# Optimization experiments

Measured on AMD Instinct MI355X. Metric: run time of the kernel, lower is better.

The kernel has to match this reference:

```python
import jax, jax.numpy as jnp
import numpy as np

NARROW = 127.0                      # narrow int8 range [-127, 127]
ACT_SCALE = 6.0 / 127.0             # fixed stand-in for learned ActQuant per-tensor scale
FLOW_SCALE = 3.96875 / 127.0        # ConstFlowQuant: max_val 3.96875, 8-bit narrow


def ste_round(x):
    # straight-through rounding (Brevitas-style)
    return x + jax.lax.stop_gradient(jnp.round(x) - x)


def act_quant(x, scale):
    # per-tensor narrow int8 fake-quant (quantize -> clamp -> dequantize)
    return scale * jnp.clip(ste_round(x / scale), -NARROW, NARROW)


def weight_quant(w):
    # per-tensor stats-based narrow int8 weight fake-quant
    s = jax.lax.stop_gradient(jnp.max(jnp.abs(w))) / NARROW + 1e-12
    return s * jnp.clip(ste_round(w / s), -NARROW, NARROW)


def conv2d(x, w, b, groups=1, pad=0):
    y = jax.lax.conv_general_dilated(
        x, w, window_strides=(1, 1), padding=[(pad, pad), (pad, pad)],
        dimension_numbers=("NCHW", "OIHW", "NCHW"), feature_group_count=groups)
    return y + b[None, :, None, None]


def setup_inputs() -> dict:
    key = jax.random.key(0)
    ks = jax.random.split(key, 12)
    B, H, W = 8, 120, 160
    cor_planes = 4 * (2 * 3 + 1) ** 2  # 196
    return {
        "flow": jax.random.normal(ks[0], (B, 2, H, W), jnp.float32),
        "corr": jax.random.normal(ks[1], (B, cor_planes, H, W), jnp.float32),
        "Wc1": jax.random.normal(ks[2], (96, cor_planes, 1, 1), jnp.float32) * 0.05,
        "bc1": jax.random.normal(ks[3], (96,), jnp.float32) * 0.05,
        "Wf1": jax.random.normal(ks[4], (64, 2, 1, 1), jnp.float32) * 0.05,
        "bf1": jax.random.normal(ks[5], (64,), jnp.float32) * 0.05,
        "Wf2": jax.random.normal(ks[6], (32, 64, 1, 1), jnp.float32) * 0.05,
        "bf2": jax.random.normal(ks[7], (32,), jnp.float32) * 0.05,
        "Wd": jax.random.normal(ks[8], (128, 1, 3, 3), jnp.float32) * 0.05,
        "bd": jax.random.normal(ks[9], (128,), jnp.float32) * 0.05,
        "Wp": jax.random.normal(ks[10], (80, 128, 1, 1), jnp.float32) * 0.05,
        "bp": jax.random.normal(ks[11], (80,), jnp.float32) * 0.05,
    }


def reference(flow, corr, Wc1, bc1, Wf1, bf1, Wf2, bf2, Wd, bd, Wp, bp):
    # convc1: 1x1 quant conv with output ActQuant, then ReLU
    cor = jax.nn.relu(act_quant(conv2d(corr, weight_quant(Wc1), bc1), ACT_SCALE))
    # convf1: 1x1 quant conv (no output quant), ReLU
    flo = jax.nn.relu(conv2d(flow, weight_quant(Wf1), bf1))
    # convf2: input ActQuant, 1x1 conv, output quant (shared with convc1), ReLU
    flo = jax.nn.relu(act_quant(conv2d(act_quant(flo, ACT_SCALE), weight_quant(Wf2), bf2), ACT_SCALE))
    # QuantCat with ConstFlowQuant on inputs and output -> [B,128,H,W]
    cor_flo = act_quant(
        jnp.concatenate([act_quant(cor, FLOW_SCALE), act_quant(flo, FLOW_SCALE)], axis=1),
        FLOW_SCALE)
    # depthwise 3x3 quant conv (groups=128), input ActQuant
    d = conv2d(act_quant(cor_flo, ACT_SCALE), weight_quant(Wd), bd, groups=128, pad=1)
    # pointwise 1x1 quant conv, input ActQuant, ReLU
    out = jax.nn.relu(conv2d(act_quant(d, ACT_SCALE), weight_quant(Wp), bp))
    # final QuantCat(out, flow) with ConstFlowQuant -> [B,82,H,W]
    return act_quant(
        jnp.concatenate([act_quant(out, FLOW_SCALE), act_quant(flow, FLOW_SCALE)], axis=1),
        FLOW_SCALE)
```

## Files before the change

kernel.cpp:

```cpp
#include <hip/hip_runtime.h>
#include <hip/hip_bf16.h>
#include <cstddef>

#define BB   8
#define HH   120
#define WW   160
#define HW   19200
#define NPIX 153600
#define CORC 196

#define AS_  ((float)(6.0/127.0))
#define FS_  0.03125f

#define OFF_WF1 18832
#define OFF_WF2 18960
#define OFF_WD  21008
#define OFF_WPQ_US 44320
#define CFQ_BYTE_OFF 131072

typedef __attribute__((ext_vector_type(8)))  short short8;
typedef __attribute__((ext_vector_type(4)))  float f32x4;

__device__ __forceinline__ float clip127(float x) {
    return fminf(fmaxf(x, -127.f), 127.f);
}

__device__ __forceinline__ unsigned short f2bf(float x) {
    unsigned int u = __float_as_uint(x);
    unsigned int r = (u + 0x7fffu + ((u >> 16) & 1u)) >> 16;
    return (unsigned short)r;
}

__global__ __launch_bounds__(256) void quant_weights(
    const float* __restrict__ Wc1, const float* __restrict__ Wf1,
    const float* __restrict__ Wf2, const float* __restrict__ Wd,
    const float* __restrict__ Wp,  float* __restrict__ ws)
{
    __shared__ float red[256];
    const int t = blockIdx.x;
    const float* src = (t == 0) ? Wc1 : (t == 1) ? Wf1 : (t == 2) ? Wf2 : (t == 3) ? Wd : Wp;
    const int n = (t == 0) ? 18816 : (t == 1) ? 128 : (t == 2) ? 2048 : (t == 3) ? 1152 : 10240;
    const int tid = threadIdx.x;

    float m = 0.f;
    for (int i = tid; i < n; i += 256) m = fmaxf(m, fabsf(src[i]));
    red[tid] = m;
    __syncthreads();
    for (int s = 128; s > 0; s >>= 1) {
        if (tid < s) red[tid] = fmaxf(red[tid], red[tid + s]);
        __syncthreads();
    }
    const float s = red[0] / 127.0f + 1e-12f;

    if (t == 0) {
        unsigned short* bf = (unsigned short*)ws + 32;
        for (int j = tid; j < 21504; j += 256) {
            const int e    = j & 7;
            const int l    = (j >> 3) & 63;
            const int tile = j >> 9;
            const int nt   = tile % 6;
            const int kt   = tile / 6;
            const int out  = nt * 16 + (l & 15);
            const int k    = kt * 32 + ((l >> 4) << 3) + e;
            float q = 0.f;
            if (k < 196) q = clip127(rintf(Wc1[out * 196 + k] / s));
            bf[j] = f2bf(q);
        }
        if (tid == 0) ws[2] = s;
    } else if (t == 4) {
        unsigned short* bf = (unsigned short*)ws + OFF_WPQ_US;
        for (int j = tid; j < 10240; j += 256) {
            const int e    = j & 7;
            const int l    = (j >> 3) & 63;
            const int tile = j >> 9;
            const int nt   = tile % 5;
            const int kt   = tile / 5;
            const int o    = nt * 16 + (l & 15);
            const int k    = kt * 32 + ((l >> 4) << 3) + e;
            const float q  = clip127(rintf(Wp[o * 128 + k] / s));
            bf[j] = f2bf(q);
        }
        if (tid == 0) ws[1] = s;
    } else {
        for (int i = tid; i < n; i += 256) {
            const float q = clip127(rintf(src[i] / s));
            if (t == 1) {
                ws[OFF_WF1 + i] = s * q;
            } else if (t == 2) {
                int o = i / 64, c = i % 64;
                ws[OFF_WF2 + c * 32 + o] = s * q;
            } else {
                ws[OFF_WD + i] = q;
            }
        }
        if (tid == 0 && t == 3) ws[0] = s;
    }
}

#define LDSTRIDE 232
__global__ __launch_bounds__(256) void k1_convc1(
    const float* __restrict__ corr, const float* __restrict__ bc1,
    const float* __restrict__ ws,   signed char* __restrict__ cfq)
{
    __shared__ unsigned short hbuf[64 * LDSTRIDE];
    __shared__ unsigned short lbuf[64 * LDSTRIDE];

    const int tid = threadIdx.x;
    const int p0  = blockIdx.x * 64;
    const int b   = p0 / HW;
    const int hw0 = p0 % HW;
    const float* cp = corr + (size_t)b * CORC * HW + hw0;

    const int pix  = tid & 63;
    const int cgrp = tid >> 6;
    unsigned short* hrow = hbuf + pix * LDSTRIDE;
    unsigned short* lrow = lbuf + pix * LDSTRIDE;

    for (int iter = 0; iter < 13; ++iter) {
        const int c0 = iter * 16 + cgrp * 4;
        unsigned long long hp = 0ull, lp = 0ull;
#pragma unroll
        for (int j = 0; j < 4; ++j) {
            const int c = c0 + j;
            float a = 0.f;
            if (c < 196) a = cp[(size_t)c * HW + pix];
            const unsigned short h = f2bf(a);
            const float hf = __uint_as_float((unsigned int)h << 16);
            const unsigned short lo = f2bf(a - hf);
            hp |= (unsigned long long)h  << (16 * j);
            lp |= (unsigned long long)lo << (16 * j);
        }
        *(unsigned long long*)(hrow + c0) = hp;
        *(unsigned long long*)(lrow + c0) = lp;
    }
    {
        const int c0z = 208 + cgrp * 4;
        *(unsigned long long*)(hrow + c0z) = 0ull;
        *(unsigned long long*)(lrow + c0z) = 0ull;
    }
    __syncthreads();

    const int w = tid >> 6;
    const int l = tid & 63;
    const int arow = w * 16 + (l & 15);
    const int koff = (l >> 4) << 3;
    const unsigned short* hA = hbuf + arow * LDSTRIDE + koff;
    const unsigned short* lA = lbuf + arow * LDSTRIDE + koff;
    const short8* Bfr = (const short8*)((const unsigned short*)ws + 32);

    f32x4 ac0 = {0.f,0.f,0.f,0.f}, ac1 = ac0, ac2 = ac0, ac3 = ac0, ac4 = ac0, ac5 = ac0;

#define NTSTEP(ACC, KT, NT)                                                      \
    {   short8 bq = Bfr[((KT) * 6 + (NT)) * 64 + l];                             \
        ACC = __builtin_amdgcn_mfma_f32_16x16x32_bf16(al_, bq, ACC, 0, 0, 0);    \
        ACC = __builtin_amdgcn_mfma_f32_16x16x32_bf16(ah_, bq, ACC, 0, 0, 0);    }

#pragma unroll
    for (int kt = 0; kt < 7; ++kt) {
        short8 ah_ = *(const short8*)(hA + kt * 32);
        short8 al_ = *(const short8*)(lA + kt * 32);
        NTSTEP(ac0, kt, 0) NTSTEP(ac1, kt, 1) NTSTEP(ac2, kt, 2)
        NTSTEP(ac3, kt, 3) NTSTEP(ac4, kt, 4) NTSTEP(ac5, kt, 5)
    }
#undef NTSTEP

    const float sc1 = ws[2];
    __syncthreads();
    signed char* t8 = (signed char*)hbuf;

#define EPI(ACC, NT)                                                             \
    {   const int out = (NT) * 16 + (l & 15);                                    \
        const float bias = bc1[out];                                             \
        _Pragma("unroll")                                                        \
        for (int i = 0; i < 4; ++i) {                                            \
            const int prow = w * 16 + ((l >> 4) << 2) + i;                       \
            float v  = fmaf(sc1, ACC[i], bias);                                  \
            float aq = AS_ * clip127(rintf(v / AS_));                            \
            float r  = fmaxf(aq, 0.f);                                           \
            float kk = fminf(rintf(r * 32.f), 127.f);                            \
            float cf = kk * FS_;                                                 \
            float q8 = clip127(rintf(cf / AS_));                                 \
            t8[out * 64 + prow] = (signed char)(int)q8;                          \
        }                                                                        }
    EPI(ac0, 0) EPI(ac1, 1) EPI(ac2, 2) EPI(ac3, 3) EPI(ac4, 4) EPI(ac5, 5)
#undef EPI
    __syncthreads();

    const unsigned int* t32 = (const unsigned int*)t8;
#pragma unroll
    for (int r = 0; r < 6; ++r) {
        const int d   = r * 256 + tid;
        const int out = d >> 4;
        const int pd  = d & 15;
        *(unsigned int*)(cfq + (size_t)(b * 128 + out) * HW + hw0 + pd * 4) = t32[d];
    }
}

typedef __attribute__((ext_vector_type(16))) float f32x16;
__global__ __launch_bounds__(256) void k1_flo(
    const float* __restrict__ flow, const float* __restrict__ bf1,
    const float* __restrict__ bf2,  const float* __restrict__ ws,
    signed char* __restrict__ cfq)
{
    const int p  = blockIdx.x * 256 + threadIdx.x;
    const int b  = p / HW;
    const int hw = p % HW;

    const float f0 = flow[(size_t)(b * 2) * HW + hw];
    const float f1 = flow[(size_t)(b * 2 + 1) * HW + hw];

    f32x16 a2a, a2b;
#pragma unroll
    for (int j = 0; j < 16; ++j) { a2a[j] = 0.f; a2b[j] = 0.f; }

    for (int c = 0; c < 64; ++c) {
        const float w0 = ws[OFF_WF1 + 2 * c];
        const float w1 = ws[OFF_WF1 + 2 * c + 1];
        float v  = fmaf(f0, w0, fmaf(f1, w1, bf1[c]));
        float r  = fmaxf(v, 0.f);
        float af = AS_ * fminf(rintf(r / AS_), 127.f);
        const float* w2 = ws + OFF_WF2 + c * 32;
#pragma unroll
        for (int j = 0; j < 16; ++j) {
            a2a[j] = fmaf(af, w2[j],      a2a[j]);
            a2b[j] = fmaf(af, w2[16 + j], a2b[j]);
        }
    }

    signed char* op = cfq + (size_t)b * 128 * HW + (size_t)96 * HW + hw;
#define FLOEPI(ACC, BASE)                                                        \
    _Pragma("unroll")                                                            \
    for (int j = 0; j < 16; ++j) {                                               \
        const int o = (BASE) + j;                                                \
        float v  = ACC[j] + bf2[o];                                              \
        float aq = AS_ * clip127(rintf(v / AS_));                                \
        float r  = fmaxf(aq, 0.f);                                               \
        float kk = fminf(rintf(r * 32.f), 127.f);                                \
        float cf = kk * FS_;                                                     \
        float q8 = clip127(rintf(cf / AS_));                                     \
        op[(size_t)o * HW] = (signed char)(int)q8;                               \
    }
    FLOEPI(a2a, 0) FLOEPI(a2b, 16)
#undef FLOEPI
}

#define STG_STRIDE 44
__global__ __launch_bounds__(256) void k2_dwpw(
    const float* __restrict__ flow, const float* __restrict__ bd,
    const float* __restrict__ bp,   const float* __restrict__ ws,
    const signed char* __restrict__ cfq, float* __restrict__ out)
{
    __shared__ signed char stage[4 * 128 * STG_STRIDE];
    __shared__ unsigned short afrag[64 * 136];

    const int tid = threadIdx.x;
    const int bid = blockIdx.x;
    const int b   = bid / 300;
    const int rem = bid % 300;
    const int h0  = (rem / 5) * 2;
    const int w0  = (rem % 5) * 32;

    for (int j = tid; j < 5120; j += 256) {
        const int i   = j % 10;
        const int c   = (j / 10) % 128;
        const int row = j / 1280;
        const int h   = h0 - 1 + row;
        const int wb  = w0 - 4 + 4 * i;
        unsigned int v = 0u;
        if (h >= 0 && h < HH && wb >= 0 && wb <= WW - 4)
            v = *(const unsigned int*)(cfq + ((size_t)(b * 128 + c) * HW + (size_t)h * WW + wb));
        *(unsigned int*)(stage + (row * 128 + c) * STG_STRIDE + i * 4) = v;
    }
    __syncthreads();

    const int c0 = tid & 63;
    const int pg = tid >> 6;
    const float sd = ws[0], sp = ws[1];
    const float ASsd = AS_ * sd;

    float wd0[9], wd1[9];
#pragma unroll
    for (int t9 = 0; t9 < 9; ++t9) {
        wd0[t9] = ws[OFF_WD + c0 * 9 + t9];
        wd1[t9] = ws[OFF_WD + (c0 + 64) * 9 + t9];
    }
    const float bd0 = bd[c0], bd1 = bd[c0 + 64];

#pragma unroll
    for (int pp = 0; pp < 16; ++pp) {
        const int pix = pg * 16 + pp;
        const int r   = pix >> 5;
        const int col = pix & 31;
        float s0 = 0.f, s1 = 0.f;
#pragma unroll
        for (int dy = 0; dy < 3; ++dy) {
            const int rb = (r + dy) * 128;
            const int xb = 3 + col;
#pragma unroll
            for (int dd = 0; dd < 3; ++dd) {
                s0 = fmaf((float)stage[(rb + c0     ) * STG_STRIDE + xb + dd], wd0[dy * 3 + dd], s0);
                s1 = fmaf((float)stage[(rb + c0 + 64) * STG_STRIDE + xb + dd], wd1[dy * 3 + dd], s1);
            }
        }
        const float q0 = clip127(rintf(fmaf(ASsd, s0, bd0) / AS_));
        const float q1 = clip127(rintf(fmaf(ASsd, s1, bd1) / AS_));
        afrag[pix * 136 + c0]      = f2bf(q0);
        afrag[pix * 136 + c0 + 64] = f2bf(q1);
    }
    __syncthreads();

    const int wv = tid >> 6;
    const int l  = tid & 63;
    const unsigned short* A = afrag + (size_t)(wv * 16 + (l & 15)) * 136 + ((l >> 4) << 3);
    const short8* Bfr = (const short8*)((const unsigned short*)ws + OFF_WPQ_US);

    f32x4 pc0 = {0.f,0.f,0.f,0.f}, pc1 = pc0, pc2 = pc0, pc3 = pc0, pc4 = pc0;

#define PTSTEP(ACC, KT, NT)                                                      \
    {   short8 bq = Bfr[((KT) * 5 + (NT)) * 64 + l];                             \
        ACC = __builtin_amdgcn_mfma_f32_16x16x32_bf16(a_, bq, ACC, 0, 0, 0);     }
#pragma unroll
    for (int kt = 0; kt < 4; ++kt) {
        short8 a_ = *(const short8*)(A + kt * 32);
        PTSTEP(pc0, kt, 0) PTSTEP(pc1, kt, 1) PTSTEP(pc2, kt, 2)
        PTSTEP(pc3, kt, 3) PTSTEP(pc4, kt, 4)
    }
#undef PTSTEP

    const float ASsp = AS_ * sp;
    float* ob = out + (size_t)b * 82 * HW;

#define PEPI(ACC, NT)                                                            \
    {   const int o = (NT) * 16 + (l & 15);                                      \
        const float bias = bp[o];                                                \
        _Pragma("unroll")                                                        \
        for (int i = 0; i < 4; ++i) {                                            \
            const int pix = wv * 16 + ((l >> 4) << 2) + i;                       \
            const int hw  = (h0 + (pix >> 5)) * WW + w0 + (pix & 31);            \
            float v = fmaf(ASsp, ACC[i], bias);                                  \
            float r = fmaxf(v, 0.f);                                             \
            float k = fminf(rintf(r * 32.f), 127.f);                             \
            ob[(size_t)o * HW + hw] = k * FS_;                                   \
        }                                                                        }
    PEPI(pc0, 0) PEPI(pc1, 1) PEPI(pc2, 2) PEPI(pc3, 3) PEPI(pc4, 4)
#undef PEPI

    if (tid < 128) {
        const int ch  = tid >> 6;
        const int pix = tid & 63;
        const int hw  = (h0 + (pix >> 5)) * WW + w0 + (pix & 31);
        const float f = flow[(size_t)(b * 2 + ch) * HW + hw];
        const float k = clip127(rintf(f * 32.f));
        ob[(size_t)(80 + ch) * HW + hw] = k * FS_;
    }
}

extern "C" void kernel_launch(void* const* d_in, const int* in_sizes, int n_in,
                              void* d_out, int out_size, void* d_ws, size_t ws_size,
                              hipStream_t stream) {
    const float* flow = (const float*)d_in[0];
    const float* corr = (const float*)d_in[1];
    const float* Wc1  = (const float*)d_in[2];
    const float* bc1  = (const float*)d_in[3];
    const float* Wf1  = (const float*)d_in[4];
    const float* bf1  = (const float*)d_in[5];
    const float* Wf2  = (const float*)d_in[6];
    const float* bf2  = (const float*)d_in[7];
    const float* Wd   = (const float*)d_in[8];
    const float* bd   = (const float*)d_in[9];
    const float* Wp   = (const float*)d_in[10];
    const float* bp   = (const float*)d_in[11];

    float* ws = (float*)d_ws;
    signed char* cfq = (signed char*)d_ws + CFQ_BYTE_OFF;
    float* out = (float*)d_out;

    quant_weights<<<5, 256, 0, stream>>>(Wc1, Wf1, Wf2, Wd, Wp, ws);
    k1_convc1<<<NPIX / 64, 256, 0, stream>>>(corr, bc1, ws, cfq);
    k1_flo<<<NPIX / 256, 256, 0, stream>>>(flow, bf1, bf2, ws, cfq);
    k2_dwpw<<<2400, 256, 0, stream>>>(flow, bd, bp, ws, cfq, out);
}
```

Measured before the change: 179.6 us.

## Load corr directly into MFMA A-fragments and double pixels per block

The convc1 kernel no longer stages the split bf16 hi/lo corr tile in LDS. Each lane loads its A-fragment elements straight from global memory into registers. Each block now covers 128 pixels, with every wave handling two 16-row tiles that share the B fragments, and it uses a small LDS buffer only for the int8 output transpose. This removes about 59KB of LDS and a barrier, which raises occupancy and halves the grid. The cost is strided, less coalesced global loads per lane and more accumulator registers.

```diff
diff --git a/kernel.cpp b/kernel.cpp
--- a/kernel.cpp
+++ b/kernel.cpp
@@ -97,102 +97,86 @@
     }
 }
 
-#define LDSTRIDE 232
-__global__ __launch_bounds__(256) void k1_convc1(
+#define TSTRIDE 136
+__global__ __launch_bounds__(256, 4) void k1_convc1(
     const float* __restrict__ corr, const float* __restrict__ bc1,
     const float* __restrict__ ws,   signed char* __restrict__ cfq)
 {
-    __shared__ unsigned short hbuf[64 * LDSTRIDE];
-    __shared__ unsigned short lbuf[64 * LDSTRIDE];
+    __shared__ signed char t8[96 * TSTRIDE];
 
     const int tid = threadIdx.x;
-    const int p0  = blockIdx.x * 64;
+    const int w   = tid >> 6;
+    const int l   = tid & 63;
+    const int p0  = blockIdx.x * 128;
     const int b   = p0 / HW;
     const int hw0 = p0 % HW;
     const float* cp = corr + (size_t)b * CORC * HW + hw0;
 
-    const int pix  = tid & 63;
-    const int cgrp = tid >> 6;
-    unsigned short* hrow = hbuf + pix * LDSTRIDE;
-    unsigned short* lrow = lbuf + pix * LDSTRIDE;
-
-    for (int iter = 0; iter < 13; ++iter) {
-        const int c0 = iter * 16 + cgrp * 4;
-        unsigned long long hp = 0ull, lp = 0ull;
-#pragma unroll
-        for (int j = 0; j < 4; ++j) {
-            const int c = c0 + j;
-            float a = 0.f;
-            if (c < 196) a = cp[(size_t)c * HW + pix];
-            const unsigned short h = f2bf(a);
-            const float hf = __uint_as_float((unsigned int)h << 16);
-            const unsigned short lo = f2bf(a - hf);
-            hp |= (unsigned long long)h  << (16 * j);
-            lp |= (unsigned long long)lo << (16 * j);
-        }
-        *(unsigned long long*)(hrow + c0) = hp;
-        *(unsigned long long*)(lrow + c0) = lp;
-    }
-    {
-        const int c0z = 208 + cgrp * 4;
-        *(unsigned long long*)(hrow + c0z) = 0ull;
-        *(unsigned long long*)(lrow + c0z) = 0ull;
-    }
-    __syncthreads();
-
-    const int w = tid >> 6;
-    const int l = tid & 63;
-    const int arow = w * 16 + (l & 15);
+    const int r0   = w * 32 + (l & 15);
     const int koff = (l >> 4) << 3;
-    const unsigned short* hA = hbuf + arow * LDSTRIDE + koff;
-    const unsigned short* lA = lbuf + arow * LDSTRIDE + koff;
     const short8* Bfr = (const short8*)((const unsigned short*)ws + 32);
 
-    f32x4 ac0 = {0.f,0.f,0.f,0.f}, ac1 = ac0, ac2 = ac0, ac3 = ac0, ac4 = ac0, ac5 = ac0;
-
-#define NTSTEP(ACC, KT, NT)                                                      \
-    {   short8 bq = Bfr[((KT) * 6 + (NT)) * 64 + l];                             \
-        ACC = __builtin_amdgcn_mfma_f32_16x16x32_bf16(al_, bq, ACC, 0, 0, 0);    \
-        ACC = __builtin_amdgcn_mfma_f32_16x16x32_bf16(ah_, bq, ACC, 0, 0, 0);    }
+    f32x4 a00 = {0.f,0.f,0.f,0.f}, a01 = a00, a02 = a00, a03 = a00, a04 = a00, a05 = a00;
+    f32x4 a10 = a00, a11 = a00, a12 = a00, a13 = a00, a14 = a00, a15 = a00;
 
 #pragma unroll
     for (int kt = 0; kt < 7; ++kt) {
-        short8 ah_ = *(const short8*)(hA + kt * 32);
-        short8 al_ = *(const short8*)(lA + kt * 32);
-        NTSTEP(ac0, kt, 0) NTSTEP(ac1, kt, 1) NTSTEP(ac2, kt, 2)
-        NTSTEP(ac3, kt, 3) NTSTEP(ac4, kt, 4) NTSTEP(ac5, kt, 5)
-    }
+        short8 h0_, l0_, h1_, l1_;
+#pragma unroll
+        for (int e = 0; e < 8; ++e) {
+            const int c = kt * 32 + koff + e;
+            float v0 = 0.f, v1 = 0.f;
+            if (c < CORC) {
+                const float* pc = cp + (size_t)c * HW;
+                v0 = pc[r0];
+                v1 = pc[r0 + 16];
+            }
+            const unsigned short h0 = f2bf(v0);
+            const unsigned short h1 = f2bf(v1);
+            h0_[e] = (short)h0;
+            h1_[e] = (short)h1;
+            l0_[e] = (short)f2bf(v0 - __uint_as_float((unsigned int)h0 << 16));
+            l1_[e] = (short)f2bf(v1 - __uint_as_float((unsigned int)h1 << 16));
+        }
+#define NTSTEP(A0, A1, NT)                                                        \
+        {   short8 bq = Bfr[((kt) * 6 + (NT)) * 64 + l];                          \
+            A0 = __builtin_amdgcn_mfma_f32_16x16x32_bf16(l0_, bq, A0, 0, 0, 0);   \
+            A0 = __builtin_amdgcn_mfma_f32_16x16x32_bf16(h0_, bq, A0, 0, 0, 0);   \
+            A1 = __builtin_amdgcn_mfma_f32_16x16x32_bf16(l1_, bq, A1, 0, 0, 0);   \
+            A1 = __builtin_amdgcn_mfma_f32_16x16x32_bf16(h1_, bq, A1, 0, 0, 0);   }
+        NTSTEP(a00, a10, 0) NTSTEP(a01, a11, 1) NTSTEP(a02, a12, 2)
+        NTSTEP(a03, a13, 3) NTSTEP(a04, a14, 4) NTSTEP(a05, a15, 5)
 #undef NTSTEP
+    }
 
     const float sc1 = ws[2];
-    __syncthreads();
-    signed char* t8 = (signed char*)hbuf;
-
-#define EPI(ACC, NT)                                                             \
-    {   const int out = (NT) * 16 + (l & 15);                                    \
-        const float bias = bc1[out];                                             \
-        _Pragma("unroll")                                                        \
-        for (int i = 0; i < 4; ++i) {                                            \
-            const int prow = w * 16 + ((l >> 4) << 2) + i;                       \
-            float v  = fmaf(sc1, ACC[i], bias);                                  \
-            float aq = AS_ * clip127(rintf(v / AS_));                            \
-            float r  = fmaxf(aq, 0.f);                                           \
-            float kk = fminf(rintf(r * 32.f), 127.f);                            \
-            float cf = kk * FS_;                                                 \
-            float q8 = clip127(rintf(cf / AS_));                                 \
-            t8[out * 64 + prow] = (signed char)(int)q8;                          \
-        }                                                                        }
-    EPI(ac0, 0) EPI(ac1, 1) EPI(ac2, 2) EPI(ac3, 3) EPI(ac4, 4) EPI(ac5, 5)
+
+#define EPI(ACC, NT, TILE)                                                        \
+    {   const int out = (NT) * 16 + (l & 15);                                     \
+        const float bias = bc1[out];                                              \
+        _Pragma("unroll")                                                         \
+        for (int i = 0; i < 4; ++i) {                                             \
+            const int prow = w * 32 + (TILE) * 16 + ((l >> 4) << 2) + i;          \
+            float v  = fmaf(sc1, ACC[i], bias);                                   \
+            float aq = AS_ * clip127(rintf(v / AS_));                             \
+            float r  = fmaxf(aq, 0.f);                                            \
+            float kk = fminf(rintf(r * 32.f), 127.f);                             \
+            float cf = kk * FS_;                                                  \
+            float q8 = clip127(rintf(cf / AS_));                                  \
+            t8[out * TSTRIDE + prow] = (signed char)(int)q8;                      \
+        }                                                                         }
+    EPI(a00, 0, 0) EPI(a01, 1, 0) EPI(a02, 2, 0) EPI(a03, 3, 0) EPI(a04, 4, 0) EPI(a05, 5, 0)
+    EPI(a10, 0, 1) EPI(a11, 1, 1) EPI(a12, 2, 1) EPI(a13, 3, 1) EPI(a14, 4, 1) EPI(a15, 5, 1)
 #undef EPI
     __syncthreads();
 
-    const unsigned int* t32 = (const unsigned int*)t8;
-#pragma unroll
-    for (int r = 0; r < 6; ++r) {
+#pragma unroll
+    for (int r = 0; r < 12; ++r) {
         const int d   = r * 256 + tid;
-        const int out = d >> 4;
-        const int pd  = d & 15;
-        *(unsigned int*)(cfq + (size_t)(b * 128 + out) * HW + hw0 + pd * 4) = t32[d];
+        const int out = d >> 5;
+        const int pd  = d & 31;
+        const unsigned int v = *(const unsigned int*)(t8 + out * TSTRIDE + pd * 4);
+        *(unsigned int*)(cfq + (size_t)(b * 128 + out) * HW + hw0 + pd * 4) = v;
     }
 }
 
@@ -376,7 +360,7 @@
     float* out = (float*)d_out;
 
     quant_weights<<<5, 256, 0, stream>>>(Wc1, Wf1, Wf2, Wd, Wp, ws);
-    k1_convc1<<<NPIX / 64, 256, 0, stream>>>(corr, bc1, ws, cfq);
+    k1_convc1<<<NPIX / 128, 256, 0, stream>>>(corr, bc1, ws, cfq);
     k1_flo<<<NPIX / 256, 256, 0, stream>>>(flow, bf1, bf2, ws, cfq);
     k2_dwpw<<<2400, 256, 0, stream>>>(flow, bd, bp, ws, cfq, out);
 }
```

New measurement: 159.7 us. -11.1%, faster.
